# Kernel tuning notes

Hardware: AMD Instinct MI355X
Metric: run time of the kernel (lower is better)

## Reference

```python
import jax, jax.numpy as jnp
import numpy as np

D_MODEL = 1024
HEAD = 16
D_K = D_MODEL // HEAD


def setup_inputs() -> dict:
    key = jax.random.key(0)
    ks = jax.random.split(key, 11)
    B, S = 2, 2048
    scale = 1.0 / np.sqrt(D_MODEL)
    inp = {
        "q": jax.random.normal(ks[0], (B, S, D_MODEL), dtype=jnp.float32),
        "k": jax.random.normal(ks[1], (B, S, D_MODEL), dtype=jnp.float32),
        "v": jax.random.normal(ks[2], (B, S, D_MODEL), dtype=jnp.float32),
        "wq": jax.random.normal(ks[3], (D_MODEL, D_MODEL), dtype=jnp.float32) * scale,
        "bq": jnp.zeros((D_MODEL,), dtype=jnp.float32),
        "wk": jax.random.normal(ks[4], (D_MODEL, D_MODEL), dtype=jnp.float32) * scale,
        "bk": jnp.zeros((D_MODEL,), dtype=jnp.float32),
        "wv": jax.random.normal(ks[5], (D_MODEL, D_MODEL), dtype=jnp.float32) * scale,
        "bv": jnp.zeros((D_MODEL,), dtype=jnp.float32),
        "wo": jax.random.normal(ks[6], (D_MODEL, D_MODEL), dtype=jnp.float32) * scale,
        "bo": jnp.zeros((D_MODEL,), dtype=jnp.float32),
    }
    return inp


def reference(q, k, v, wq, bq, wk, bk, wv, bv, wo, bo):
    B, S, _ = q.shape
    # linear projections, split into heads: [B, H, S, Dk]
    def proj(x, w, b):
        y = x @ w.T + b
        return y.reshape(B, -1, HEAD, D_K).transpose(0, 2, 1, 3)

    qh, kh, vh = proj(q, wq, bq), proj(k, wk, bk), proj(v, wv, bv)
    # scaled dot-product attention (dropout = identity in eval)
    scores = jnp.einsum("bhqd,bhkd->bhqk", qh, kh) / jnp.sqrt(jnp.float32(D_K))
    probs = jax.nn.softmax(scores, axis=-1)
    ctx = jnp.einsum("bhqk,bhkd->bhqd", probs, vh)
    concat = ctx.transpose(0, 2, 1, 3).reshape(B, S, D_MODEL)
    return concat @ wo.T + bo
```

## Files before the change

### kernel.cpp

```cpp
#include <hip/hip_runtime.h>
#include <stdint.h>

#define S_LEN 2048
#define NH 16
#define DK 64
#define DMODEL 1024

typedef __attribute__((ext_vector_type(8))) _Float16 half8;
typedef __attribute__((ext_vector_type(4))) _Float16 half4;
typedef __attribute__((ext_vector_type(4))) float f32x4;
typedef __attribute__((ext_vector_type(16))) float f32x16;
typedef __attribute__((ext_vector_type(4))) uint32_t u32x4;

#define OFF_QX   0u
#define OFF_KX   4194304u
#define OFF_VX   8388608u
#define OFF_WQ   12582912u
#define OFF_WK   13631488u
#define OFF_WV   14680064u
#define OFF_WO   15728640u
#define OFF_QH   16777216u
#define OFF_KH   20971520u
#define OFF_VH   25165824u
#define OFF_CTX  29360128u

#define LOG2E 1.44269504088896340736f
#define SOFT_M 10.0f

__device__ __forceinline__ f32x4 mfma_f16(half8 a, half8 b, f32x4 c) {
  return __builtin_amdgcn_mfma_f32_16x16x32_f16(a, b, c, 0, 0, 0);
}
__device__ __forceinline__ f32x16 mfma32(half8 a, half8 b, f32x16 c) {
  return __builtin_amdgcn_mfma_f32_32x32x16_f16(a, b, c, 0, 0, 0);
}

__device__ __forceinline__ void gload16(const void* g, void* l) {
  __builtin_amdgcn_global_load_lds(
      (const __attribute__((address_space(1))) uint32_t*)g,
      (__attribute__((address_space(3))) uint32_t*)l, 16, 0, 0);
}

__device__ __forceinline__ uint32_t pkrtz(float a, float b) {
  auto pk2 = __builtin_amdgcn_cvt_pkrtz(a, b);
  return __builtin_bit_cast(uint32_t, pk2);
}

__global__ void cast_f32_f16(const float* __restrict__ q, const float* __restrict__ k,
                             const float* __restrict__ v, const float* __restrict__ wq,
                             const float* __restrict__ wk, const float* __restrict__ wv,
                             const float* __restrict__ wo, _Float16* __restrict__ ws16) {
  const int seg = blockIdx.y;
  const float* src;
  unsigned n, doff;
  switch (seg) {
    case 0: src = q;  n = 4194304u; doff = OFF_QX; break;
    case 1: src = k;  n = 4194304u; doff = OFF_KX; break;
    case 2: src = v;  n = 4194304u; doff = OFF_VX; break;
    case 3: src = wq; n = 1048576u; doff = OFF_WQ; break;
    case 4: src = wk; n = 1048576u; doff = OFF_WK; break;
    case 5: src = wv; n = 1048576u; doff = OFF_WV; break;
    default: src = wo; n = 1048576u; doff = OFF_WO; break;
  }
  unsigned i = (blockIdx.x * 256u + threadIdx.x) * 4u;
  if (i >= n) return;
  float4 f = *(const float4*)(src + i);
  half4 h;
  h.x = (_Float16)f.x; h.y = (_Float16)f.y; h.z = (_Float16)f.z; h.w = (_Float16)f.w;
  *(half4*)(ws16 + doff + i) = h;
}

__global__ __launch_bounds__(256, 3) void gemm_qkv(
    _Float16* __restrict__ ws16, const float* __restrict__ bq,
    const float* __restrict__ bk, const float* __restrict__ bv) {
  const int t = threadIdx.x;
  const int w = t >> 6, lane = t & 63, l16 = lane & 15, quad = lane >> 4;
  const int wx = w & 1, wy = w >> 1;
  const int bx = blockIdx.x;
  const int which = bx >> 3;
  const int n0 = (bx & 7) * 128;
  const int m0 = blockIdx.y * 128;

  const _Float16* A  = ws16 + (which == 0 ? OFF_QX : which == 1 ? OFF_KX : OFF_VX);
  const _Float16* Bt = ws16 + (which == 0 ? OFF_WQ : which == 1 ? OFF_WK : OFF_WV);
  const float* bias  = (which == 0) ? bq : (which == 1) ? bk : bv;
  _Float16* dst      = ws16 + (which == 0 ? OFF_QH : which == 1 ? OFF_KH : OFF_VH);
  const float scale  = (which == 0) ? 0.125f * LOG2E : 1.0f;

  __shared__ _Float16 smem[2][128][64];
  _Float16 (*As)[64] = smem[0];
  _Float16 (*Bs)[64] = smem[1];

  f32x4 zero = {0.f, 0.f, 0.f, 0.f};
  f32x4 acc[4][4];
#pragma unroll
  for (int i = 0; i < 4; i++)
#pragma unroll
    for (int j = 0; j < 4; j++) acc[i][j] = zero;

  const int lr = lane >> 3;
  const int gch = (lane & 7) ^ lr;
  const _Float16* gA[4];
  const _Float16* gB[4];
  _Float16* lA[4];
  _Float16* lB[4];
#pragma unroll
  for (int j = 0; j < 4; j++) {
    int n = w * 4 + j;
    gA[j] = A + (size_t)(m0 + n * 8 + lr) * DMODEL + gch * 8;
    gB[j] = Bt + (size_t)(n0 + n * 8 + lr) * DMODEL + gch * 8;
    lA[j] = &As[n * 8][0];
    lB[j] = &Bs[n * 8][0];
  }
  const int xr = l16 & 7;
  const int c0 = (quad ^ xr) * 8;
  const int c1 = ((4 + quad) ^ xr) * 8;

  for (int k0 = 0; k0 < DMODEL; k0 += 64) {
    __syncthreads();
#pragma unroll
    for (int j = 0; j < 4; j++) {
      gload16(gA[j] + k0, lA[j]);
      gload16(gB[j] + k0, lB[j]);
    }
    __syncthreads();

    half8 af[2][4], bf[2][4];
#pragma unroll
    for (int i = 0; i < 4; i++) {
      af[0][i] = *(const half8*)&As[wy * 64 + i * 16 + l16][c0];
      af[1][i] = *(const half8*)&As[wy * 64 + i * 16 + l16][c1];
      bf[0][i] = *(const half8*)&Bs[wx * 64 + i * 16 + l16][c0];
      bf[1][i] = *(const half8*)&Bs[wx * 64 + i * 16 + l16][c1];
    }
#pragma unroll
    for (int s = 0; s < 2; s++)
#pragma unroll
      for (int i = 0; i < 4; i++)
#pragma unroll
        for (int j = 0; j < 4; j++)
          acc[i][j] = mfma_f16(af[s][i], bf[s][j], acc[i][j]);
  }

  if (which == 2) {
#pragma unroll
    for (int j = 0; j < 4; j++) {
      int n = n0 + wx * 64 + j * 16 + l16;
      float bn = bias[n];
      int h = n >> 6, d = n & 63;
#pragma unroll
      for (int i = 0; i < 4; i++) {
        int m = m0 + wy * 64 + i * 16 + quad * 4;
        int b = m >> 11, s = m & 2047;
        half4 hv;
#pragma unroll
        for (int r = 0; r < 4; r++) hv[r] = (_Float16)(acc[i][j][r] + bn);
        *(half4*)(dst + ((size_t)(b * NH + h) * DK + d) * S_LEN + s) = hv;
      }
    }
  } else {
    _Float16* Cs = &smem[0][0][0];
    __syncthreads();
#pragma unroll
    for (int j = 0; j < 4; j++) {
      int n = wx * 64 + j * 16 + l16;
      float bn = bias[n0 + n];
      int cl = n >> 3, nb = n & 7;
#pragma unroll
      for (int i = 0; i < 4; i++) {
#pragma unroll
        for (int r = 0; r < 4; r++) {
          int m = wy * 64 + i * 16 + quad * 4 + r;
          int cp = cl ^ (m & 15);
          Cs[m * 128 + cp * 8 + nb] = (_Float16)((acc[i][j][r] + bn) * scale);
        }
      }
    }
    __syncthreads();
#pragma unroll
    for (int p = 0; p < 8; p++) {
      int row = (t >> 4) + p * 16;
      int cl = t & 15;
      int cp = cl ^ (row & 15);
      half8 v = *(const half8*)&Cs[row * 128 + cp * 8];
      int m = m0 + row;
      int b = m >> 11, s = m & 2047;
      int ng = n0 + cl * 8;
      int h = ng >> 6, d = ng & 63;
      *(half8*)(dst + ((size_t)(b * NH + h) * S_LEN + s) * DK + d) = v;
    }
  }
}

__global__ __launch_bounds__(256, 2) void attn(_Float16* __restrict__ ws16) {
  const int t = threadIdx.x;
  const int w = t >> 6, lane = t & 63;
  const int l32 = lane & 31, hi = lane >> 5;
  const int wg = blockIdx.y * 16 + blockIdx.x;
  const int xcd = wg & 7, ix = wg >> 3;
  const int bh = (xcd << 2) | (ix >> 4);
  const int q0 = (ix & 15) * 128 + w * 32;

  const _Float16* Qh  = ws16 + OFF_QH + (size_t)bh * S_LEN * DK;
  const _Float16* Kh  = ws16 + OFF_KH + (size_t)bh * S_LEN * DK;
  const _Float16* VhT = ws16 + OFF_VH + (size_t)bh * DK * S_LEN;
  _Float16* ctx = ws16 + OFF_CTX;

  __shared__ _Float16 Ks[2][64][64];
  __shared__ _Float16 Vt[2][64][64];

  half8 qb[4];
#pragma unroll
  for (int c = 0; c < 4; c++)
    qb[c] = *(const half8*)(Qh + (size_t)(q0 + l32) * DK + c * 16 + hi * 8);

  f32x16 o_acc[2];
#pragma unroll
  for (int dt = 0; dt < 2; dt++)
#pragma unroll
    for (int r = 0; r < 16; r++) o_acc[dt][r] = 0.f;
  float ls[4] = {0.f, 0.f, 0.f, 0.f};

  f32x16 minit;
#pragma unroll
  for (int r = 0; r < 16; r++) minit[r] = -SOFT_M;

  const int lr = lane >> 3;
  const int gch = (lane & 7) ^ lr;
  const _Float16* gk0 = Kh + (size_t)(w * 8 + lr) * DK + gch * 8;
  const _Float16* gk1 = Kh + (size_t)(32 + w * 8 + lr) * DK + gch * 8;
  const _Float16* gv0 = VhT + (size_t)(w * 8 + lr) * S_LEN + gch * 8;
  const _Float16* gv1 = VhT + (size_t)(32 + w * 8 + lr) * S_LEN + gch * 8;

  const int sw = l32 & 7;

  gload16(gk0, &Ks[0][w * 8][0]);
  gload16(gk1, &Ks[0][32 + w * 8][0]);
  gload16(gv0, &Vt[0][w * 8][0]);
  gload16(gv1, &Vt[0][32 + w * 8][0]);
  __syncthreads();

  for (int kt2 = 0; kt2 < 16; kt2++) {
#pragma unroll
    for (int h = 0; h < 2; h++) {
      const int kt = kt2 * 2 + h;
      const int cur = h;

      if (kt < 31) {
        const int kb = (kt + 1) * 64;
        gload16(gk0 + (size_t)kb * DK, &Ks[cur ^ 1][w * 8][0]);
        gload16(gk1 + (size_t)kb * DK, &Ks[cur ^ 1][32 + w * 8][0]);
        gload16(gv0 + kb, &Vt[cur ^ 1][w * 8][0]);
        gload16(gv1 + kb, &Vt[cur ^ 1][32 + w * 8][0]);
      }
      __builtin_amdgcn_sched_barrier(0);

#pragma unroll
      for (int ktile = 0; ktile < 2; ktile++) {
        const int krow = ktile * 32 + l32;
        f32x16 sc = minit;
        __builtin_amdgcn_s_setprio(1);
#pragma unroll
        for (int c = 0; c < 4; c++) {
          half8 af = *(const half8*)&Ks[cur][krow][((2 * c + hi) ^ sw) * 8];
          sc = mfma32(af, qb[c], sc);
        }
        __builtin_amdgcn_s_setprio(0);

        float pv[16];
#pragma unroll
        for (int i = 0; i < 16; i++) {
          pv[i] = __builtin_amdgcn_exp2f(sc[i]);
          ls[i & 3] += pv[i];
        }
        uint32_t wd[8];
#pragma unroll
        for (int j = 0; j < 8; j++) {
          wd[j] = pkrtz(pv[2 * j], pv[2 * j + 1]);
        }
        asm("v_permlane32_swap_b32 %0, %1" : "+v"(wd[0]), "+v"(wd[2]));
        asm("v_permlane32_swap_b32 %0, %1" : "+v"(wd[1]), "+v"(wd[3]));
        asm("v_permlane32_swap_b32 %0, %1" : "+v"(wd[4]), "+v"(wd[6]));
        asm("v_permlane32_swap_b32 %0, %1" : "+v"(wd[5]), "+v"(wd[7]));
        u32x4 aw0 = {wd[0], wd[1], wd[2], wd[3]};
        u32x4 aw1 = {wd[4], wd[5], wd[6], wd[7]};
        half8 ap0 = __builtin_bit_cast(half8, aw0);
        half8 ap1 = __builtin_bit_cast(half8, aw1);

        __builtin_amdgcn_s_setprio(1);
#pragma unroll
        for (int dt = 0; dt < 2; dt++) {
          const int drow = dt * 32 + l32;
          f32x16 c = o_acc[dt];
          c = mfma32(ap0, *(const half8*)&Vt[cur][drow][((2 * (ktile * 2 + 0) + hi) ^ sw) * 8], c);
          c = mfma32(ap1, *(const half8*)&Vt[cur][drow][((2 * (ktile * 2 + 1) + hi) ^ sw) * 8], c);
          o_acc[dt] = c;
        }
        __builtin_amdgcn_s_setprio(0);
      }

      __syncthreads();
    }
  }

  float lsum = (ls[0] + ls[1]) + (ls[2] + ls[3]);
  lsum += __shfl_xor(lsum, 32);
  float inv = 1.0f / lsum;

  const int b = bh >> 4, hh = bh & 15;
#pragma unroll
  for (int r = 0; r < 16; r++) {
    int qloc = (r & 3) + 8 * (r >> 2) + 4 * hi;
    float iv = __shfl(inv, qloc);
    int sq = q0 + qloc;
    size_t base = ((size_t)(b * S_LEN + sq)) * DMODEL + hh * DK + l32;
    ctx[base] = (_Float16)(o_acc[0][r] * iv);
    ctx[base + 32] = (_Float16)(o_acc[1][r] * iv);
  }
}

__global__ __launch_bounds__(256, 3) void gemm_out(
    const _Float16* __restrict__ ws16, const float* __restrict__ bo,
    float* __restrict__ out) {
  const int t = threadIdx.x;
  const int w = t >> 6, lane = t & 63, l16 = lane & 15, quad = lane >> 4;
  const int wx = w & 1, wy = w >> 1;
  const int n0 = blockIdx.x * 128;
  const int m0 = blockIdx.y * 128;

  const _Float16* A = ws16 + OFF_CTX;
  const _Float16* Bt = ws16 + OFF_WO;

  __shared__ _Float16 As[128][64];
  __shared__ _Float16 Bs[128][64];

  f32x4 zero = {0.f, 0.f, 0.f, 0.f};
  f32x4 acc[4][4];
#pragma unroll
  for (int i = 0; i < 4; i++)
#pragma unroll
    for (int j = 0; j < 4; j++) acc[i][j] = zero;

  const int lr = lane >> 3;
  const int gch = (lane & 7) ^ lr;
  const _Float16* gA[4];
  const _Float16* gB[4];
  _Float16* lA[4];
  _Float16* lB[4];
#pragma unroll
  for (int j = 0; j < 4; j++) {
    int n = w * 4 + j;
    gA[j] = A + (size_t)(m0 + n * 8 + lr) * DMODEL + gch * 8;
    gB[j] = Bt + (size_t)(n0 + n * 8 + lr) * DMODEL + gch * 8;
    lA[j] = &As[n * 8][0];
    lB[j] = &Bs[n * 8][0];
  }
  const int xr = l16 & 7;
  const int c0 = (quad ^ xr) * 8;
  const int c1 = ((4 + quad) ^ xr) * 8;

  for (int k0 = 0; k0 < DMODEL; k0 += 64) {
    __syncthreads();
#pragma unroll
    for (int j = 0; j < 4; j++) {
      gload16(gA[j] + k0, lA[j]);
      gload16(gB[j] + k0, lB[j]);
    }
    __syncthreads();

    half8 af[2][4], bf[2][4];
#pragma unroll
    for (int i = 0; i < 4; i++) {
      af[0][i] = *(const half8*)&As[wy * 64 + i * 16 + l16][c0];
      af[1][i] = *(const half8*)&As[wy * 64 + i * 16 + l16][c1];
      bf[0][i] = *(const half8*)&Bs[wx * 64 + i * 16 + l16][c0];
      bf[1][i] = *(const half8*)&Bs[wx * 64 + i * 16 + l16][c1];
    }
#pragma unroll
    for (int s = 0; s < 2; s++)
#pragma unroll
      for (int i = 0; i < 4; i++)
#pragma unroll
        for (int j = 0; j < 4; j++)
          acc[i][j] = mfma_f16(af[s][i], bf[s][j], acc[i][j]);
  }

#pragma unroll
  for (int j = 0; j < 4; j++) {
    int n = n0 + wx * 64 + j * 16 + l16;
    float bn = bo[n];
#pragma unroll
    for (int i = 0; i < 4; i++) {
#pragma unroll
      for (int r = 0; r < 4; r++) {
        int m = m0 + wy * 64 + i * 16 + quad * 4 + r;
        out[(size_t)m * DMODEL + n] = acc[i][j][r] + bn;
      }
    }
  }
}

extern "C" void kernel_launch(void* const* d_in, const int* in_sizes, int n_in,
                              void* d_out, int out_size, void* d_ws, size_t ws_size,
                              hipStream_t stream) {
  const float* q  = (const float*)d_in[0];
  const float* k  = (const float*)d_in[1];
  const float* v  = (const float*)d_in[2];
  const float* wq = (const float*)d_in[3];
  const float* bq = (const float*)d_in[4];
  const float* wk = (const float*)d_in[5];
  const float* bk = (const float*)d_in[6];
  const float* wv = (const float*)d_in[7];
  const float* bv = (const float*)d_in[8];
  const float* wo = (const float*)d_in[9];
  const float* bo = (const float*)d_in[10];
  float* out = (float*)d_out;
  _Float16* ws16 = (_Float16*)d_ws;

  cast_f32_f16<<<dim3(4096, 7), 256, 0, stream>>>(q, k, v, wq, wk, wv, wo, ws16);
  gemm_qkv<<<dim3(24, 32), 256, 0, stream>>>(ws16, bq, bk, bv);
  attn<<<dim3(16, 32), 256, 0, stream>>>(ws16);
  gemm_out<<<dim3(8, 32), 256, 0, stream>>>(ws16, bo, out);
}
```

Before: 224.3 us.

## Split attention key range across two wave groups with shared-memory reduction

Each attention block now runs 512 threads: two halves of four waves, each half covering 1024 of the 2048 keys for the same 128 queries. The partial outputs and row sums are combined through shared memory before normalisation and the ctx write. This halves the serial key loop per wave and doubles the waves per CU, aiming to hide latency better in the softmax/MFMA loop. In exchange it doubles LDS use per block, adds a final reduction step with a barrier, and leaves half the waves idle during the epilogue.

```diff
diff --git a/kernel.cpp b/kernel.cpp
--- a/kernel.cpp
+++ b/kernel.cpp
@@ -191,22 +191,24 @@
   }
 }
 
-__global__ __launch_bounds__(256, 2) void attn(_Float16* __restrict__ ws16) {
+__global__ __launch_bounds__(512, 4) void attn(_Float16* __restrict__ ws16) {
   const int t = threadIdx.x;
   const int w = t >> 6, lane = t & 63;
   const int l32 = lane & 31, hi = lane >> 5;
+  const int half = w & 1;
+  const int qg = w >> 1;
   const int wg = blockIdx.y * 16 + blockIdx.x;
   const int xcd = wg & 7, ix = wg >> 3;
   const int bh = (xcd << 2) | (ix >> 4);
-  const int q0 = (ix & 15) * 128 + w * 32;
+  const int q0 = (ix & 15) * 128 + qg * 32;
 
   const _Float16* Qh  = ws16 + OFF_QH + (size_t)bh * S_LEN * DK;
   const _Float16* Kh  = ws16 + OFF_KH + (size_t)bh * S_LEN * DK;
   const _Float16* VhT = ws16 + OFF_VH + (size_t)bh * DK * S_LEN;
   _Float16* ctx = ws16 + OFF_CTX;
 
-  __shared__ _Float16 Ks[2][64][64];
-  __shared__ _Float16 Vt[2][64][64];
+  __shared__ _Float16 Ks[2][2][64][64];
+  __shared__ _Float16 Vt[2][2][64][64];
 
   half8 qb[4];
 #pragma unroll
@@ -226,31 +228,32 @@
 
   const int lr = lane >> 3;
   const int gch = (lane & 7) ^ lr;
-  const _Float16* gk0 = Kh + (size_t)(w * 8 + lr) * DK + gch * 8;
-  const _Float16* gk1 = Kh + (size_t)(32 + w * 8 + lr) * DK + gch * 8;
-  const _Float16* gv0 = VhT + (size_t)(w * 8 + lr) * S_LEN + gch * 8;
-  const _Float16* gv1 = VhT + (size_t)(32 + w * 8 + lr) * S_LEN + gch * 8;
+  const int kvbase = half * 1024;
+  const _Float16* gk0 = Kh + (size_t)(kvbase + qg * 8 + lr) * DK + gch * 8;
+  const _Float16* gk1 = Kh + (size_t)(kvbase + 32 + qg * 8 + lr) * DK + gch * 8;
+  const _Float16* gv0 = VhT + (size_t)(qg * 8 + lr) * S_LEN + kvbase + gch * 8;
+  const _Float16* gv1 = VhT + (size_t)(32 + qg * 8 + lr) * S_LEN + kvbase + gch * 8;
 
   const int sw = l32 & 7;
 
-  gload16(gk0, &Ks[0][w * 8][0]);
-  gload16(gk1, &Ks[0][32 + w * 8][0]);
-  gload16(gv0, &Vt[0][w * 8][0]);
-  gload16(gv1, &Vt[0][32 + w * 8][0]);
+  gload16(gk0, &Ks[0][half][qg * 8][0]);
+  gload16(gk1, &Ks[0][half][32 + qg * 8][0]);
+  gload16(gv0, &Vt[0][half][qg * 8][0]);
+  gload16(gv1, &Vt[0][half][32 + qg * 8][0]);
   __syncthreads();
 
-  for (int kt2 = 0; kt2 < 16; kt2++) {
+  for (int kt2 = 0; kt2 < 8; kt2++) {
 #pragma unroll
     for (int h = 0; h < 2; h++) {
       const int kt = kt2 * 2 + h;
       const int cur = h;
 
-      if (kt < 31) {
+      if (kt < 15) {
         const int kb = (kt + 1) * 64;
-        gload16(gk0 + (size_t)kb * DK, &Ks[cur ^ 1][w * 8][0]);
-        gload16(gk1 + (size_t)kb * DK, &Ks[cur ^ 1][32 + w * 8][0]);
-        gload16(gv0 + kb, &Vt[cur ^ 1][w * 8][0]);
-        gload16(gv1 + kb, &Vt[cur ^ 1][32 + w * 8][0]);
+        gload16(gk0 + (size_t)kb * DK, &Ks[cur ^ 1][half][qg * 8][0]);
+        gload16(gk1 + (size_t)kb * DK, &Ks[cur ^ 1][half][32 + qg * 8][0]);
+        gload16(gv0 + kb, &Vt[cur ^ 1][half][qg * 8][0]);
+        gload16(gv1 + kb, &Vt[cur ^ 1][half][32 + qg * 8][0]);
       }
       __builtin_amdgcn_sched_barrier(0);
 
@@ -261,7 +264,7 @@
         __builtin_amdgcn_s_setprio(1);
 #pragma unroll
         for (int c = 0; c < 4; c++) {
-          half8 af = *(const half8*)&Ks[cur][krow][((2 * c + hi) ^ sw) * 8];
+          half8 af = *(const half8*)&Ks[cur][half][krow][((2 * c + hi) ^ sw) * 8];
           sc = mfma32(af, qb[c], sc);
         }
         __builtin_amdgcn_s_setprio(0);
@@ -291,8 +294,8 @@
         for (int dt = 0; dt < 2; dt++) {
           const int drow = dt * 32 + l32;
           f32x16 c = o_acc[dt];
-          c = mfma32(ap0, *(const half8*)&Vt[cur][drow][((2 * (ktile * 2 + 0) + hi) ^ sw) * 8], c);
-          c = mfma32(ap1, *(const half8*)&Vt[cur][drow][((2 * (ktile * 2 + 1) + hi) ^ sw) * 8], c);
+          c = mfma32(ap0, *(const half8*)&Vt[cur][half][drow][((2 * (ktile * 2 + 0) + hi) ^ sw) * 8], c);
+          c = mfma32(ap1, *(const half8*)&Vt[cur][half][drow][((2 * (ktile * 2 + 1) + hi) ^ sw) * 8], c);
           o_acc[dt] = c;
         }
         __builtin_amdgcn_s_setprio(0);
@@ -304,17 +307,36 @@
 
   float lsum = (ls[0] + ls[1]) + (ls[2] + ls[3]);
   lsum += __shfl_xor(lsum, 32);
-  float inv = 1.0f / lsum;
-
-  const int b = bh >> 4, hh = bh & 15;
-#pragma unroll
-  for (int r = 0; r < 16; r++) {
-    int qloc = (r & 3) + 8 * (r >> 2) + 4 * hi;
-    float iv = __shfl(inv, qloc);
-    int sq = q0 + qloc;
-    size_t base = ((size_t)(b * S_LEN + sq)) * DMODEL + hh * DK + l32;
-    ctx[base] = (_Float16)(o_acc[0][r] * iv);
-    ctx[base + 32] = (_Float16)(o_acc[1][r] * iv);
+
+  float* red = (float*)&Ks[0][0][0][0];
+  if (half == 1) {
+#pragma unroll
+    for (int dt = 0; dt < 2; dt++)
+#pragma unroll
+      for (int r = 0; r < 16; r++)
+        red[((qg * 2 + dt) * 16 + r) * 64 + lane] = o_acc[dt][r];
+    red[8192 + qg * 64 + lane] = lsum;
+  }
+  __syncthreads();
+  if (half == 0) {
+    lsum += red[8192 + qg * 64 + lane];
+#pragma unroll
+    for (int dt = 0; dt < 2; dt++)
+#pragma unroll
+      for (int r = 0; r < 16; r++)
+        o_acc[dt][r] += red[((qg * 2 + dt) * 16 + r) * 64 + lane];
+    float inv = 1.0f / lsum;
+
+    const int b = bh >> 4, hh = bh & 15;
+#pragma unroll
+    for (int r = 0; r < 16; r++) {
+      int qloc = (r & 3) + 8 * (r >> 2) + 4 * hi;
+      float iv = __shfl(inv, qloc);
+      int sq = q0 + qloc;
+      size_t base = ((size_t)(b * S_LEN + sq)) * DMODEL + hh * DK + l32;
+      ctx[base] = (_Float16)(o_acc[0][r] * iv);
+      ctx[base + 32] = (_Float16)(o_acc[1][r] * iv);
+    }
   }
 }
 
@@ -418,6 +440,6 @@
 
   cast_f32_f16<<<dim3(4096, 7), 256, 0, stream>>>(q, k, v, wq, wk, wv, wo, ws16);
   gemm_qkv<<<dim3(24, 32), 256, 0, stream>>>(ws16, bq, bk, bv);
-  attn<<<dim3(16, 32), 256, 0, stream>>>(ws16);
+  attn<<<dim3(16, 32), 512, 0, stream>>>(ws16);
   gemm_out<<<dim3(8, 32), 256, 0, stream>>>(ws16, bo, out);
 }
```

Result: no change. 226.2 us (+0.9%).
